# Kernel tuning notes

Measured on AMD Instinct MI355X. Metric: run time of the kernel, lower is better.

Reference implementation:

```python
import jax, jax.numpy as jnp
import numpy as np

D_MODEL = 512
NHEAD = 8
MAX_REL = 256  # max_relative_position


def _linear(x, w, b):
    # torch nn.Linear: y = x @ W^T + b, W: [out, in]
    return jnp.einsum('...i,oi->...o', x, w) + b


def setup_inputs() -> dict:
    key = jax.random.key(0)
    ks = jax.random.split(key, 16)
    B, S, D = 32, 512, D_MODEL
    s = 0.02
    inp = {
        'query': jax.random.normal(ks[0], (B, S, D), jnp.float32),
        'key':   jax.random.normal(ks[1], (B, S, D), jnp.float32),
        'value': jax.random.normal(ks[2], (B, S, D), jnp.float32),
        # local attention projections (torch Linear weights [out,in])
        'wq': jax.random.normal(ks[3], (D, D), jnp.float32) * s,
        'bq': jnp.zeros((D,), jnp.float32),
        'wk': jax.random.normal(ks[4], (D, D), jnp.float32) * s,
        'bk': jnp.zeros((D,), jnp.float32),
        'wv': jax.random.normal(ks[5], (D, D), jnp.float32) * s,
        'bv': jnp.zeros((D,), jnp.float32),
        'wo': jax.random.normal(ks[6], (D, D), jnp.float32) * s,
        'bo': jnp.zeros((D,), jnp.float32),
        # relative-position key embedding table [2*MAX_REL+1, head_dim]
        'rel_k': jax.random.normal(ks[7], (2 * MAX_REL + 1, D // NHEAD), jnp.float32) * s,
        # global nn.MultiheadAttention (nhead//2 heads): packed in_proj + out_proj
        'g_in_w': jax.random.normal(ks[8], (3 * D, D), jnp.float32) * s,
        'g_in_b': jnp.zeros((3 * D,), jnp.float32),
        'g_out_w': jax.random.normal(ks[9], (D, D), jnp.float32) * s,
        'g_out_b': jnp.zeros((D,), jnp.float32),
    }
    return inp


def reference(query, key, value, wq, bq, wk, bk, wv, bv, wo, bo, rel_k,
              g_in_w, g_in_b, g_out_w, g_out_b):
    B, S, D = query.shape
    H, hd = NHEAD, D // NHEAD

    # --- local attention with relative-position bias ---
    q = _linear(query, wq, bq).reshape(B, S, H, hd).transpose(0, 2, 1, 3)  # [B,H,S,hd]
    k = _linear(key,   wk, bk).reshape(B, S, H, hd).transpose(0, 2, 1, 3)
    v = _linear(value, wv, bv).reshape(B, S, H, hd).transpose(0, 2, 1, 3)

    scores = jnp.einsum('bhqd,bhkd->bhqk', q, k) / jnp.sqrt(jnp.float32(hd))

    # relative positions: distance[i,j] = j - i, clamped, shifted to [0, 2*MAX_REL]
    idx = jnp.arange(S)
    rel_ids = jnp.clip(idx[None, :] - idx[:, None], -MAX_REL, MAX_REL) + MAX_REL  # [S,S]
    rel_pos_k = rel_k[rel_ids]  # [S, S, hd]
    scores = scores + jnp.einsum('bhld,lrd->bhlr', q, rel_pos_k)

    attn = jax.nn.softmax(scores, axis=-1)
    local = jnp.einsum('bhqk,bhkd->bhqd', attn, v)
    local = local.transpose(0, 2, 1, 3).reshape(B, S, D)

    # --- global MHA with H//2 heads ---
    Hg = H // 2
    hdg = D // Hg
    qg = _linear(query, g_in_w[:D], g_in_b[:D]).reshape(B, S, Hg, hdg).transpose(0, 2, 1, 3)
    kg = _linear(key,   g_in_w[D:2 * D], g_in_b[D:2 * D]).reshape(B, S, Hg, hdg).transpose(0, 2, 1, 3)
    vg = _linear(value, g_in_w[2 * D:], g_in_b[2 * D:]).reshape(B, S, Hg, hdg).transpose(0, 2, 1, 3)
    gs = jnp.einsum('bhqd,bhkd->bhqk', qg, kg) / jnp.sqrt(jnp.float32(hdg))
    ga = jax.nn.softmax(gs, axis=-1)
    g = jnp.einsum('bhqk,bhkd->bhqd', ga, vg).transpose(0, 2, 1, 3).reshape(B, S, D)
    g = _linear(g, g_out_w, g_out_b)

    combined = 0.7 * local + 0.3 * g
    return _linear(combined, wo, bo)
```

## Files before the change

kernel.cpp:

```cpp
#include <hip/hip_runtime.h>

typedef __attribute__((ext_vector_type(8))) short bh8;
typedef __attribute__((ext_vector_type(4))) float f4;

#define DEVI static __device__ __forceinline__

DEVI unsigned short f2b(float f) {
  union { float f; unsigned u; } v; v.f = f;
  unsigned r = v.u + 0x7fffu + ((v.u >> 16) & 1u);
  return (unsigned short)(r >> 16);
}
DEVI float b2f(unsigned short h) {
  union { unsigned u; float f; } v; v.u = ((unsigned)h) << 16;
  return v.f;
}
DEVI f4 mfma16(bh8 a, bh8 b, f4 c) {
  return __builtin_amdgcn_mfma_f32_16x16x32_bf16(a, b, c, 0, 0, 0);
}
DEVI void gload_lds16(const unsigned short* g, unsigned short* l) {
  __builtin_amdgcn_global_load_lds(
      (const __attribute__((address_space(1))) void*)(g),
      (__attribute__((address_space(3))) void*)(l), 16, 0, 0);
}

__global__ __launch_bounds__(256) void prep_all_kern(
    const float* __restrict__ q, const float* __restrict__ k, const float* __restrict__ v,
    const float* __restrict__ wq, const float* __restrict__ wk, const float* __restrict__ wv,
    const float* __restrict__ g_in_w, const float* __restrict__ g_out_w,
    const float* __restrict__ wo, const float* __restrict__ rel_k,
    const float* __restrict__ bgo, const float* __restrict__ bo,
    unsigned short* __restrict__ xq, unsigned short* __restrict__ xk, unsigned short* __restrict__ xv,
    unsigned short* __restrict__ Wq, unsigned short* __restrict__ Wk, unsigned short* __restrict__ Wv,
    unsigned short* __restrict__ Wo_, unsigned short* __restrict__ WgoT,
    unsigned short* __restrict__ Bfin, unsigned short* __restrict__ Rk,
    float* __restrict__ bias2) {
  if (blockIdx.x < 8192) {
    long i = ((long)blockIdx.x * 256 + threadIdx.x) * 4;
    float4 a = *(const float4*)(q + i);
    float4 b = *(const float4*)(k + i);
    float4 c = *(const float4*)(v + i);
    union { unsigned short s[4]; uint2 u; } pa, pb, pc;
    pa.s[0] = f2b(a.x); pa.s[1] = f2b(a.y); pa.s[2] = f2b(a.z); pa.s[3] = f2b(a.w);
    pb.s[0] = f2b(b.x); pb.s[1] = f2b(b.y); pb.s[2] = f2b(b.z); pb.s[3] = f2b(b.w);
    pc.s[0] = f2b(c.x); pc.s[1] = f2b(c.y); pc.s[2] = f2b(c.z); pc.s[3] = f2b(c.w);
    *(uint2*)(xq + i) = pa.u;
    *(uint2*)(xk + i) = pb.u;
    *(uint2*)(xv + i) = pc.u;
    return;
  }
  int bw = blockIdx.x - 8192;
  if (bw >= 2337) {
    int o = (bw - 2337) * 256 + threadIdx.x;
    if (o < 512) {
      const float* r = wo + (long)o * 512;
      float s = 0.f;
#pragma unroll 4
      for (int m = 0; m < 512; m += 4) {
        float4 a = *(const float4*)(r + m);
        float4 b = *(const float4*)(bgo + m);
        s += a.x * b.x + a.y * b.y + a.z * b.z + a.w * b.w;
      }
      bias2[o] = bo[o] + 0.3f * s;
    }
    return;
  }
  long i = ((long)bw * 256 + threadIdx.x) * 4;
  if (i >= 2392128L) return;
  if (i >= 2097152L && i < 2359296L) {
    long off = i - 2097152L;
    int ii = (int)(off >> 9), p = (int)(off & 511);
    union { unsigned short s[4]; uint2 u; } w;
#pragma unroll
    for (int tt = 0; tt < 4; tt++) w.s[tt] = f2b(g_out_w[(p + tt) * 512 + ii]);
    *(uint2*)(WgoT + off) = w.u;
    return;
  }
  const float* src; unsigned short* dst; long off; float sc = 1.0f;
  if (i < 524288L)        { dst = Wq;  off = i; src = (i < 262144L) ? wq + i : g_in_w + (i - 262144L); }
  else if (i < 1048576L)  { long j = i - 524288L;  dst = Wk;  off = j; src = (j < 262144L) ? wk + j : g_in_w + j; }
  else if (i < 1572864L)  { long j = i - 1048576L; dst = Wv;  off = j; src = (j < 262144L) ? wv + j : g_in_w + 262144L + j; }
  else if (i < 1835008L)  { long j = i - 1572864L; dst = Wo_; off = j; src = wo + j; }
  else if (i < 2097152L)  { long j = i - 1835008L; int col = (int)(j >> 9), kk = (int)(j & 511);
                            dst = Bfin; off = (long)col * 1024 + kk; src = wo + j; sc = 0.7f; }
  else                    { long j = i - 2359296L; dst = Rk;  off = j; src = rel_k + j; }
  float4 f = *(const float4*)src;
  union { unsigned short s[4]; uint2 u; } p;
  p.s[0] = f2b(f.x * sc); p.s[1] = f2b(f.y * sc); p.s[2] = f2b(f.z * sc); p.s[3] = f2b(f.w * sc);
  *(uint2*)(dst + off) = p.u;
}

__global__ __launch_bounds__(256) void gemm3_kern(
    const unsigned short* __restrict__ Xq, const unsigned short* __restrict__ Xk,
    const unsigned short* __restrict__ Xv,
    const unsigned short* __restrict__ Wq, const unsigned short* __restrict__ Wk,
    const unsigned short* __restrict__ Wv,
    const float* __restrict__ bq, const float* __restrict__ bk, const float* __restrict__ bv,
    const float* __restrict__ g_in_b,
    unsigned short* __restrict__ Yq, unsigned short* __restrict__ Yk_,
    unsigned short* __restrict__ Yvt_l, unsigned short* __restrict__ Yvt_g,
    const unsigned short* __restrict__ Wo_, const unsigned short* __restrict__ WgoT,
    unsigned short* __restrict__ Bfin) {
  __shared__ unsigned short lsA[128 * 32];
  __shared__ unsigned short lsB[128 * 32];
  const int t = threadIdx.x;
  const int lane = t & 63, w = t >> 6;
  const int l15 = lane & 15, g = lane >> 4, g4 = g * 4;
  const int gs8 = (g ^ ((l15 >> 1) & 3)) * 8;
  const int n = blockIdx.x;

  const unsigned short *Ap, *Bp;
  const float *b0 = nullptr, *b1 = nullptr;
  int seg, rb, cb;
  if (n < 3072) {
    seg = n >> 10;
    int m = n & 1023;
    int x = m >> 3, c = m & 7;
    rb = (c * 16 + (x & 15)) * 128;
    cb = (x >> 4) * 128;
    Ap = (seg == 0) ? Xq : (seg == 1) ? Xk : Xv;
    Bp = (seg == 0) ? Wq : (seg == 1) ? Wk : Wv;
    b0 = (seg == 0) ? bq : (seg == 1) ? bk : bv;
    b1 = g_in_b + seg * 512;
  } else {
    seg = 3;
    int m2 = n - 3072;
    rb = (m2 & 3) * 128; cb = (m2 >> 2) * 128;
    Ap = Wo_; Bp = WgoT;
  }

  const int wr = (w >> 1) * 64, wc = (w & 1) * 64;
  const int r0 = t >> 2, r1 = 64 + (t >> 2);
  const int k0i = ((t & 3) ^ ((t >> 3) & 3)) * 8;

  const unsigned short* pa0 = Ap + (long)(rb + r0) * 512 + k0i;
  const unsigned short* pa1 = Ap + (long)(rb + r1) * 512 + k0i;
  const unsigned short* pb0 = Bp + (long)(cb + r0) * 512 + k0i;
  const unsigned short* pb1 = Bp + (long)(cb + r1) * 512 + k0i;
  unsigned short* dA0 = lsA + w * 512;
  unsigned short* dA1 = lsA + 2048 + w * 512;
  unsigned short* dB0 = lsB + w * 512;
  unsigned short* dB1 = lsB + 2048 + w * 512;

  f4 acc[4][4] = {};
  for (int k0 = 0; k0 < 512; k0 += 32) {
    __syncthreads();
    gload_lds16(pa0 + k0, dA0);
    gload_lds16(pa1 + k0, dA1);
    gload_lds16(pb0 + k0, dB0);
    gload_lds16(pb1 + k0, dB1);
    __syncthreads();
    bh8 af[4], bf[4];
#pragma unroll
    for (int m = 0; m < 4; m++) af[m] = *(const bh8*)(lsA + (wr + m * 16 + l15) * 32 + gs8);
#pragma unroll
    for (int nn = 0; nn < 4; nn++) bf[nn] = *(const bh8*)(lsB + (wc + nn * 16 + l15) * 32 + gs8);
    __builtin_amdgcn_s_setprio(1);
#pragma unroll
    for (int m = 0; m < 4; m++)
#pragma unroll
      for (int nn = 0; nn < 4; nn++)
        acc[m][nn] = mfma16(af[m], bf[nn], acc[m][nn]);
    __builtin_amdgcn_s_setprio(0);
  }

  if (seg == 3) {
#pragma unroll
    for (int m = 0; m < 4; m++)
#pragma unroll
      for (int nn = 0; nn < 4; nn++)
#pragma unroll
        for (int j = 0; j < 4; j++) {
          int row = rb + wr + m * 16 + g4 + j;
          int col = cb + wc + nn * 16 + l15;
          Bfin[(long)row * 1024 + 512 + col] = f2b(0.3f * acc[m][nn][j]);
        }
    return;
  }
  if (seg == 2) {
#pragma unroll
    for (int m = 0; m < 4; m++)
#pragma unroll
      for (int nn = 0; nn < 4; nn++) {
        int col = cb + wc + nn * 16 + l15;
        float bsv = (col < 512) ? b0[col] : b1[col - 512];
        unsigned r[4];
#pragma unroll
        for (int j = 0; j < 4; j++) {
          union { float f; unsigned u; } v; v.f = acc[m][nn][j] + bsv;
          r[j] = v.u + 0x7fffu + ((v.u >> 16) & 1u);
        }
        unsigned lo = (r[0] >> 16) | (r[1] & 0xffff0000u);
        unsigned hi = (r[2] >> 16) | (r[3] & 0xffff0000u);
        int row0 = rb + wr + m * 16 + g4;
        int bb = row0 >> 9, s = row0 & 511;
        if (col < 512) {
          int hh = col >> 6, d = col & 63;
          *(uint2*)(Yvt_l + (((long)(bb * 8 + hh) * 64 + d) << 9) + s) = make_uint2(lo, hi);
        } else {
          int c2 = col - 512, hg = c2 >> 7, dg = c2 & 127;
          *(uint2*)(Yvt_g + (((long)(bb * 4 + hg) * 128 + dg) << 9) + s) = make_uint2(lo, hi);
        }
      }
    return;
  }
  unsigned short* Yo = (seg == 0) ? Yq : Yk_;
#pragma unroll
  for (int m = 0; m < 4; m++)
#pragma unroll
    for (int nn = 0; nn < 4; nn++)
#pragma unroll
      for (int j = 0; j < 4; j++) {
        int row = rb + wr + m * 16 + g4 + j;
        int col = cb + wc + nn * 16 + l15;
        float v = acc[m][nn][j] + ((col < 512) ? b0[col] : b1[col - 512]);
        Yo[(long)row * 1024 + col] = f2b(v);
      }
}

__global__ __launch_bounds__(256) void gemm_fin_kern(
    const unsigned short* __restrict__ A, const unsigned short* __restrict__ Bw,
    const float* __restrict__ bias0, float* __restrict__ outf) {
  __shared__ unsigned short lsA[128 * 32];
  __shared__ unsigned short lsB[128 * 32];
  const int t = threadIdx.x;
  const int lane = t & 63, w = t >> 6;
  const int l15 = lane & 15, g = lane >> 4, g4 = g * 4;
  const int gs8 = (g ^ ((l15 >> 1) & 3)) * 8;
  int n = blockIdx.x;
  int x = n >> 3, c = n & 7;
  const int rb = (c * 16 + (x & 15)) * 128;
  const int cb = (x >> 4) * 128;
  const int wr = (w >> 1) * 64, wc = (w & 1) * 64;
  const int r0 = t >> 2, r1 = 64 + (t >> 2);
  const int k0i = ((t & 3) ^ ((t >> 3) & 3)) * 8;

  const unsigned short* pa0 = A + (long)(rb + r0) * 1024 + k0i;
  const unsigned short* pa1 = A + (long)(rb + r1) * 1024 + k0i;
  const unsigned short* pb0 = Bw + (long)(cb + r0) * 1024 + k0i;
  const unsigned short* pb1 = Bw + (long)(cb + r1) * 1024 + k0i;
  unsigned short* dA0 = lsA + w * 512;
  unsigned short* dA1 = lsA + 2048 + w * 512;
  unsigned short* dB0 = lsB + w * 512;
  unsigned short* dB1 = lsB + 2048 + w * 512;

  f4 acc[4][4] = {};
  for (int k0 = 0; k0 < 1024; k0 += 32) {
    __syncthreads();
    gload_lds16(pa0 + k0, dA0);
    gload_lds16(pa1 + k0, dA1);
    gload_lds16(pb0 + k0, dB0);
    gload_lds16(pb1 + k0, dB1);
    __syncthreads();
    bh8 af[4], bf[4];
#pragma unroll
    for (int m = 0; m < 4; m++) af[m] = *(const bh8*)(lsA + (wr + m * 16 + l15) * 32 + gs8);
#pragma unroll
    for (int nn = 0; nn < 4; nn++) bf[nn] = *(const bh8*)(lsB + (wc + nn * 16 + l15) * 32 + gs8);
    __builtin_amdgcn_s_setprio(1);
#pragma unroll
    for (int m = 0; m < 4; m++)
#pragma unroll
      for (int nn = 0; nn < 4; nn++)
        acc[m][nn] = mfma16(af[m], bf[nn], acc[m][nn]);
    __builtin_amdgcn_s_setprio(0);
  }
#pragma unroll
  for (int m = 0; m < 4; m++)
#pragma unroll
    for (int nn = 0; nn < 4; nn++)
#pragma unroll
      for (int j = 0; j < 4; j++) {
        int row = rb + wr + m * 16 + g4 + j;
        int col = cb + wc + nn * 16 + l15;
        outf[(long)row * 512 + col] = acc[m][nn][j] + bias0[col];
      }
}

__global__ __launch_bounds__(512, 4) void attn_local_kern(
    const unsigned short* __restrict__ Yq, const unsigned short* __restrict__ Yk,
    const unsigned short* __restrict__ Yvt, const unsigned short* __restrict__ relk,
    unsigned short* __restrict__ outC) {
  __shared__ unsigned short kv[2][8192];
  __shared__ unsigned short buf[32 * 524];
  __shared__ float redbuf[8][32];

  const int t = threadIdx.x, lane = t & 63, w = t >> 6;
  const int l15 = lane & 15, g = lane >> 4, g8 = g * 8;
  int n = blockIdx.x;
  int bid = (n & 7) * 512 + (n >> 3);
  const int qt = bid & 15;
  const int h = (bid >> 4) & 7;
  const int b = bid >> 7;
  const int qb = qt * 32;
  const long base = ((long)(b * 512)) * 1024 + h * 64;
  const long vbase = ((long)(b * 8 + h)) * 64 * 512;

#define STAGE_K(ROFF, BUF) { \
    const int c_ = t & 7; \
    _Pragma("unroll") \
    for (int it = 0; it < 2; it++) { \
      int rr = it * 64 + (t >> 3); \
      gload_lds16(Yk + base + (long)((ROFF) + rr) * 1024 + ((c_ ^ (rr & 7)) * 8), \
                  kv[BUF] + it * 4096 + w * 512); \
    } }
#define STAGE_V(COFF, BUF) { \
    const int c_ = t & 15; \
    _Pragma("unroll") \
    for (int it = 0; it < 2; it++) { \
      int dd_ = it * 32 + (t >> 4); \
      gload_lds16(Yvt + vbase + (long)dd_ * 512 + (COFF) + ((c_ ^ (dd_ & 15)) * 8), \
                  kv[BUF] + it * 4096 + w * 512); \
    } }
#define QK(CH) { \
    int rl = w * 16 + l15; \
    const unsigned short* kb_ = kv[(CH) & 1]; \
    bh8 k0 = *(const bh8*)(kb_ + rl * 64 + ((g ^ (rl & 7)) * 8)); \
    bh8 k1 = *(const bh8*)(kb_ + rl * 64 + (((g + 4) ^ (rl & 7)) * 8)); \
    _Pragma("unroll") \
    for (int mm = 0; mm < 2; mm++) { \
      f4 a = {}; \
      a = mfma16(qf[mm][0], k0, a); \
      a = mfma16(qf[mm][1], k1, a); \
      sc[mm][CH] = a; \
    } }
#define GATHER(CH) { \
    _Pragma("unroll") \
    for (int mm = 0; mm < 2; mm++) \
    _Pragma("unroll") \
    for (int j = 0; j < 4; j++) { \
      int lr = mm * 16 + g * 4 + j; \
      int rowb = lr * 524; \
      int idx = rowb + 256 - (qb + lr) + (CH) * 128 + w * 16 + l15; \
      idx = idx < rowb ? rowb : idx; \
      idx = idx > rowb + 512 ? rowb + 512 : idx; \
      float p = exp2f(fmaf(sc[mm][CH][j], 0.18033688011112042f, b2f(buf[idx]))); \
      sc[mm][CH][j] = p; \
      rs[mm][j] += p; \
    } }

  STAGE_K(0, 0);

  bh8 qf[2][2];
#pragma unroll
  for (int mm = 0; mm < 2; mm++) {
    const unsigned short* qp = Yq + base + (long)(qb + mm * 16 + l15) * 1024 + g8;
    qf[mm][0] = *(const bh8*)(qp);
    qf[mm][1] = *(const bh8*)(qp + 32);
  }

  for (int tt = w; tt < 33; tt += 8) {
    int ri = tt * 16 + l15; if (ri > 512) ri = 512;
    const unsigned short* rp = relk + ri * 64 + g8;
    bh8 rf0 = *(const bh8*)(rp), rf1 = *(const bh8*)(rp + 32);
    int col = tt * 16 + l15;
#pragma unroll
    for (int mm = 0; mm < 2; mm++) {
      f4 a = {};
      a = mfma16(qf[mm][0], rf0, a);
      a = mfma16(qf[mm][1], rf1, a);
      if (col < 524) {
#pragma unroll
        for (int j = 0; j < 4; j++)
          buf[(mm * 16 + g * 4 + j) * 524 + col] = f2b(a[j] * 1.4426950408889634f);
      }
    }
  }
  __syncthreads();

  f4 sc[2][4];
  float rs[2][4] = {};

#pragma unroll
  for (int c = 0; c < 4; c++) {
    if (c < 3) { STAGE_K((c + 1) * 128, (c + 1) & 1); }
    else       { STAGE_V(0, 0); }
    __builtin_amdgcn_s_setprio(1);
    QK(c);
    __builtin_amdgcn_s_setprio(0);
    GATHER(c);
    __syncthreads();
  }

#pragma unroll
  for (int mm = 0; mm < 2; mm++)
#pragma unroll
    for (int j = 0; j < 4; j++) {
      int lr = mm * 16 + g * 4 + j;
      float s = rs[mm][j];
      for (int d = 1; d < 16; d <<= 1) s += __shfl_xor(s, d, 64);
      if (l15 == 0) redbuf[w][lr] = s;
    }
#pragma unroll
  for (int mm = 0; mm < 2; mm++)
#pragma unroll
    for (int ch = 0; ch < 4; ch++) {
      int col = ch * 128 + w * 16 + l15;
#pragma unroll
      for (int j = 0; j < 4; j++)
        buf[(mm * 16 + g * 4 + j) * 524 + col] = f2b(sc[mm][ch][j]);
    }
  __syncthreads();

  const int mmw = w >> 2, dt = w & 3;
  const int dd = dt * 16 + l15;
  float rinvj[4];
#pragma unroll
  for (int j = 0; j < 4; j++) {
    int lr = mmw * 16 + g * 4 + j;
    float s = 0.f;
#pragma unroll
    for (int ww = 0; ww < 8; ww++) s += redbuf[ww][lr];
    rinvj[j] = __builtin_amdgcn_rcpf(s);
  }

  f4 accO = {};
#pragma unroll
  for (int d = 0; d < 4; d++) {
    if (d < 3) { STAGE_V((d + 1) * 128, (d + 1) & 1); }
    const unsigned short* vb_ = kv[d & 1];
    __builtin_amdgcn_s_setprio(1);
#pragma unroll
    for (int ks2 = 0; ks2 < 4; ks2++) {
      union { uint2 u[2]; bh8 v; } pa;
      const unsigned short* pp = buf + (mmw * 16 + l15) * 524 + (d * 4 + ks2) * 32 + g8;
      pa.u[0] = *(const uint2*)(pp);
      pa.u[1] = *(const uint2*)(pp + 4);
      bh8 vv = *(const bh8*)(vb_ + dd * 128 + (((ks2 * 4 + g) ^ (dd & 15)) * 8));
      accO = mfma16(pa.v, vv, accO);
    }
    __builtin_amdgcn_s_setprio(0);
    if (d < 3) __syncthreads();
  }
#pragma unroll
  for (int j = 0; j < 4; j++) {
    int row = qb + mmw * 16 + g * 4 + j;
    outC[((long)(b * 512 + row)) * 1024 + h * 64 + dt * 16 + l15] = f2b(accO[j] * rinvj[j]);
  }
#undef STAGE_K
#undef STAGE_V
#undef QK
#undef GATHER
}

__global__ __launch_bounds__(512, 4) void attn_glob_kern(
    const unsigned short* __restrict__ Yq, const unsigned short* __restrict__ Yk,
    const unsigned short* __restrict__ Yvt, unsigned short* __restrict__ outC) {
  __shared__ unsigned short kv[2][8192];
  __shared__ unsigned short buf[32 * 520];
  __shared__ float redbuf[8][32];

  const int t = threadIdx.x, lane = t & 63, w = t >> 6;
  const int l15 = lane & 15, g = lane >> 4, g8 = g * 8;
  int n = blockIdx.x;
  int bid = (n & 7) * 256 + (n >> 3);
  const int qt = bid & 15;
  const int hg = (bid >> 4) & 3;
  const int b = bid >> 6;
  const int qb = qt * 32;
  const long base = ((long)(b * 512)) * 1024 + 512 + hg * 128;
  const long vgbase = ((long)(b * 4 + hg)) * 128 * 512;

#define STAGE_GK(KC, BUF) { \
    const int c_ = t & 15; \
    _Pragma("unroll") \
    for (int it = 0; it < 2; it++) { \
      int rr = it * 32 + (t >> 4); \
      gload_lds16(Yk + base + (long)((KC) * 64 + rr) * 1024 + ((c_ ^ (rr & 15)) * 8), \
                  kv[BUF] + it * 4096 + w * 512); \
    } }
#define STAGE_GV(KC, BUF) { \
    const int c_ = t & 7; \
    _Pragma("unroll") \
    for (int it = 0; it < 2; it++) { \
      int dd_ = it * 64 + (t >> 3); \
      gload_lds16(Yvt + vgbase + (long)dd_ * 512 + (KC) * 64 + ((c_ ^ (dd_ & 7)) * 8), \
                  kv[BUF] + it * 4096 + w * 512); \
    } }

  const int mmq = w >> 2, wq4 = w & 3;

  STAGE_GK(0, 0);

  bh8 qf[4];
  {
    const unsigned short* qp = Yq + base + (long)(qb + mmq * 16 + l15) * 1024 + g8;
#pragma unroll
    for (int ks = 0; ks < 4; ks++) qf[ks] = *(const bh8*)(qp + ks * 32);
  }
  __syncthreads();

  f4 sc8[8];
#pragma unroll
  for (int kc = 0; kc < 8; kc++) {
    if (kc < 7) { STAGE_GK(kc + 1, (kc + 1) & 1); }
    else        { STAGE_GV(0, 0); }
    const unsigned short* kb_ = kv[kc & 1];
    const int rl = wq4 * 16 + l15;
    __builtin_amdgcn_s_setprio(1);
    f4 a = {};
#pragma unroll
    for (int ks = 0; ks < 4; ks++) {
      bh8 kf = *(const bh8*)(kb_ + rl * 128 + (((ks * 4 + g) ^ (rl & 15)) * 8));
      a = mfma16(qf[ks], kf, a);
    }
    sc8[kc] = a;
    __builtin_amdgcn_s_setprio(0);
    __syncthreads();
  }

#pragma unroll
  for (int j = 0; j < 4; j++) {
    int lr = mmq * 16 + g * 4 + j;
    float s = 0.f;
#pragma unroll
    for (int kc = 0; kc < 8; kc++) {
      float p = exp2f(sc8[kc][j] * 0.12751745334f);
      sc8[kc][j] = p;
      s += p;
    }
    for (int d = 1; d < 16; d <<= 1) s += __shfl_xor(s, d, 64);
    if (l15 == 0) redbuf[w][lr] = s;
  }
  __syncthreads();

#pragma unroll
  for (int kc = 0; kc < 8; kc++) {
    int col = kc * 64 + wq4 * 16 + l15;
#pragma unroll
    for (int j = 0; j < 4; j++)
      buf[(mmq * 16 + g * 4 + j) * 520 + col] = f2b(sc8[kc][j]);
  }
  float rinv[2][4];
#pragma unroll
  for (int mm = 0; mm < 2; mm++)
#pragma unroll
    for (int j = 0; j < 4; j++) {
      int lr = mm * 16 + g * 4 + j;
      float s = redbuf[mm * 4 + 0][lr] + redbuf[mm * 4 + 1][lr] +
                redbuf[mm * 4 + 2][lr] + redbuf[mm * 4 + 3][lr];
      rinv[mm][j] = __builtin_amdgcn_rcpf(s);
    }
  __syncthreads();

  const int dd = w * 16 + l15;
  f4 accO[2] = {};
#pragma unroll
  for (int kc = 0; kc < 8; kc++) {
    if (kc < 7) { STAGE_GV(kc + 1, (kc + 1) & 1); }
    const unsigned short* vb_ = kv[kc & 1];
    __builtin_amdgcn_s_setprio(1);
#pragma unroll
    for (int ks2 = 0; ks2 < 2; ks2++) {
      bh8 vv = *(const bh8*)(vb_ + dd * 64 + (((ks2 * 4 + g) ^ (dd & 7)) * 8));
#pragma unroll
      for (int mm = 0; mm < 2; mm++) {
        union { uint2 u[2]; bh8 v; } pa;
        const unsigned short* pp = buf + (mm * 16 + l15) * 520 + kc * 64 + ks2 * 32 + g8;
        pa.u[0] = *(const uint2*)(pp);
        pa.u[1] = *(const uint2*)(pp + 4);
        accO[mm] = mfma16(pa.v, vv, accO[mm]);
      }
    }
    __builtin_amdgcn_s_setprio(0);
    if (kc < 7) __syncthreads();
  }
#pragma unroll
  for (int mm = 0; mm < 2; mm++)
#pragma unroll
    for (int j = 0; j < 4; j++) {
      int row = qb + mm * 16 + g * 4 + j;
      outC[((long)(b * 512 + row)) * 1024 + 512 + hg * 128 + w * 16 + l15] = f2b(accO[mm][j] * rinv[mm][j]);
    }
#undef STAGE_GK
#undef STAGE_GV
}

extern "C" void kernel_launch(void* const* d_in, const int* in_sizes, int n_in,
                              void* d_out, int out_size, void* d_ws, size_t ws_size,
                              hipStream_t stream) {
  const float* query = (const float*)d_in[0];
  const float* key   = (const float*)d_in[1];
  const float* value = (const float*)d_in[2];
  const float* wq = (const float*)d_in[3];   const float* bq = (const float*)d_in[4];
  const float* wk = (const float*)d_in[5];   const float* bk = (const float*)d_in[6];
  const float* wv = (const float*)d_in[7];   const float* bv = (const float*)d_in[8];
  const float* wo = (const float*)d_in[9];   const float* bo = (const float*)d_in[10];
  const float* rel_k = (const float*)d_in[11];
  const float* g_in_w = (const float*)d_in[12];  const float* g_in_b = (const float*)d_in[13];
  const float* g_out_w = (const float*)d_in[14]; const float* g_out_b = (const float*)d_in[15];

  unsigned short* p = (unsigned short*)d_ws;
  unsigned short* Xq = p;            p += 8388608;
  unsigned short* Xk = p;            p += 8388608;
  unsigned short* Xv = p;            p += 8388608;
  unsigned short* Yq = p;            p += 16777216;
  unsigned short* Yk = p;            p += 16777216;
  unsigned short* Yvt_l = p;         p += 8388608;
  unsigned short* Yvt_g = p;         p += 8388608;
  unsigned short* Wq = p;            p += 524288;
  unsigned short* Wk = p;            p += 524288;
  unsigned short* Wv = p;            p += 524288;
  unsigned short* Wo_ = p;           p += 262144;
  unsigned short* WgoT = p;          p += 262144;
  unsigned short* Bfin = p;          p += 524288;
  unsigned short* Rk = p;            p += 32832;
  float* bias2 = (float*)p;          p += 1024;
  unsigned short* CAT = Xq;

  prep_all_kern<<<10531, 256, 0, stream>>>(query, key, value,
                                           wq, wk, wv, g_in_w, g_out_w, wo, rel_k,
                                           g_out_b, bo,
                                           Xq, Xk, Xv, Wq, Wk, Wv, Wo_, WgoT, Bfin, Rk, bias2);

  gemm3_kern<<<3088, 256, 0, stream>>>(Xq, Xk, Xv, Wq, Wk, Wv, bq, bk, bv, g_in_b,
                                       Yq, Yk, Yvt_l, Yvt_g, Wo_, WgoT, Bfin);

  attn_local_kern<<<4096, 512, 0, stream>>>(Yq, Yk, Yvt_l, Rk, CAT);
  attn_glob_kern<<<2048, 512, 0, stream>>>(Yq, Yk, Yvt_g, CAT);

  gemm_fin_kern<<<512, 256, 0, stream>>>(CAT, Bfin, bias2, (float*)d_out);
}
```

Baseline: 313.4 us.

## Triple-buffer GEMM K-loop loads and merge local/global attention kernels

Both GEMM kernels now use a three-stage LDS ring with direct global-to-LDS loads issued one tile ahead. A single barrier per iteration is guarded by explicit vmcnt waits, replacing the two __syncthreads around synchronous loads. Separately, the local and global attention kernels are fused into one launch that interleaves two local blocks and one global block per group of three. The aim is to hide load latency and remove a launch plus tail gap. The cost is triple the GEMM LDS use (48KB), which may lower occupancy, and a larger combined attention kernel whose register and LDS footprint is the maximum of both branches.

After: 290.0 us. 1.08x faster.

```diff
diff --git a/kernel.cpp b/kernel.cpp
--- a/kernel.cpp
+++ b/kernel.cpp
@@ -100,8 +100,8 @@
     unsigned short* __restrict__ Yvt_l, unsigned short* __restrict__ Yvt_g,
     const unsigned short* __restrict__ Wo_, const unsigned short* __restrict__ WgoT,
     unsigned short* __restrict__ Bfin) {
-  __shared__ unsigned short lsA[128 * 32];
-  __shared__ unsigned short lsB[128 * 32];
+  __shared__ unsigned short lsA[3][4096];
+  __shared__ unsigned short lsB[3][4096];
   const int t = threadIdx.x;
   const int lane = t & 63, w = t >> 6;
   const int l15 = lane & 15, g = lane >> 4, g4 = g * 4;
@@ -131,29 +131,35 @@
   const int wr = (w >> 1) * 64, wc = (w & 1) * 64;
   const int r0 = t >> 2, r1 = 64 + (t >> 2);
   const int k0i = ((t & 3) ^ ((t >> 3) & 3)) * 8;
-
   const unsigned short* pa0 = Ap + (long)(rb + r0) * 512 + k0i;
   const unsigned short* pa1 = Ap + (long)(rb + r1) * 512 + k0i;
   const unsigned short* pb0 = Bp + (long)(cb + r0) * 512 + k0i;
   const unsigned short* pb1 = Bp + (long)(cb + r1) * 512 + k0i;
-  unsigned short* dA0 = lsA + w * 512;
-  unsigned short* dA1 = lsA + 2048 + w * 512;
-  unsigned short* dB0 = lsB + w * 512;
-  unsigned short* dB1 = lsB + 2048 + w * 512;
-
+
+#define GST(KK, BUF) { \
+    gload_lds16(pa0 + (KK), lsA[BUF] + w * 512); \
+    gload_lds16(pa1 + (KK), lsA[BUF] + 2048 + w * 512); \
+    gload_lds16(pb0 + (KK), lsB[BUF] + w * 512); \
+    gload_lds16(pb1 + (KK), lsB[BUF] + 2048 + w * 512); }
+
+  GST(0, 0);
   f4 acc[4][4] = {};
-  for (int k0 = 0; k0 < 512; k0 += 32) {
-    __syncthreads();
-    gload_lds16(pa0 + k0, dA0);
-    gload_lds16(pa1 + k0, dA1);
-    gload_lds16(pb0 + k0, dB0);
-    gload_lds16(pb1 + k0, dB1);
-    __syncthreads();
+#pragma unroll
+  for (int it = 0; it < 16; it++) {
+    if (it < 15) {
+      GST((it + 1) * 32, (it + 1) % 3);
+      asm volatile("s_waitcnt vmcnt(4)" ::: "memory");
+    } else {
+      asm volatile("s_waitcnt vmcnt(0)" ::: "memory");
+    }
+    __builtin_amdgcn_s_barrier();
+    const unsigned short* LA = lsA[it % 3];
+    const unsigned short* LB = lsB[it % 3];
     bh8 af[4], bf[4];
 #pragma unroll
-    for (int m = 0; m < 4; m++) af[m] = *(const bh8*)(lsA + (wr + m * 16 + l15) * 32 + gs8);
-#pragma unroll
-    for (int nn = 0; nn < 4; nn++) bf[nn] = *(const bh8*)(lsB + (wc + nn * 16 + l15) * 32 + gs8);
+    for (int m = 0; m < 4; m++) af[m] = *(const bh8*)(LA + (wr + m * 16 + l15) * 32 + gs8);
+#pragma unroll
+    for (int nn = 0; nn < 4; nn++) bf[nn] = *(const bh8*)(LB + (wc + nn * 16 + l15) * 32 + gs8);
     __builtin_amdgcn_s_setprio(1);
 #pragma unroll
     for (int m = 0; m < 4; m++)
@@ -162,6 +168,7 @@
         acc[m][nn] = mfma16(af[m], bf[nn], acc[m][nn]);
     __builtin_amdgcn_s_setprio(0);
   }
+#undef GST
 
   if (seg == 3) {
 #pragma unroll
@@ -220,8 +227,8 @@
 __global__ __launch_bounds__(256) void gemm_fin_kern(
     const unsigned short* __restrict__ A, const unsigned short* __restrict__ Bw,
     const float* __restrict__ bias0, float* __restrict__ outf) {
-  __shared__ unsigned short lsA[128 * 32];
-  __shared__ unsigned short lsB[128 * 32];
+  __shared__ unsigned short lsA[3][4096];
+  __shared__ unsigned short lsB[3][4096];
   const int t = threadIdx.x;
   const int lane = t & 63, w = t >> 6;
   const int l15 = lane & 15, g = lane >> 4, g4 = g * 4;
@@ -238,24 +245,31 @@
   const unsigned short* pa1 = A + (long)(rb + r1) * 1024 + k0i;
   const unsigned short* pb0 = Bw + (long)(cb + r0) * 1024 + k0i;
   const unsigned short* pb1 = Bw + (long)(cb + r1) * 1024 + k0i;
-  unsigned short* dA0 = lsA + w * 512;
-  unsigned short* dA1 = lsA + 2048 + w * 512;
-  unsigned short* dB0 = lsB + w * 512;
-  unsigned short* dB1 = lsB + 2048 + w * 512;
-
+
+#define GST(KK, BUF) { \
+    gload_lds16(pa0 + (KK), lsA[BUF] + w * 512); \
+    gload_lds16(pa1 + (KK), lsA[BUF] + 2048 + w * 512); \
+    gload_lds16(pb0 + (KK), lsB[BUF] + w * 512); \
+    gload_lds16(pb1 + (KK), lsB[BUF] + 2048 + w * 512); }
+
+  GST(0, 0);
   f4 acc[4][4] = {};
-  for (int k0 = 0; k0 < 1024; k0 += 32) {
-    __syncthreads();
-    gload_lds16(pa0 + k0, dA0);
-    gload_lds16(pa1 + k0, dA1);
-    gload_lds16(pb0 + k0, dB0);
-    gload_lds16(pb1 + k0, dB1);
-    __syncthreads();
+#pragma unroll
+  for (int it = 0; it < 32; it++) {
+    if (it < 31) {
+      GST((it + 1) * 32, (it + 1) % 3);
+      asm volatile("s_waitcnt vmcnt(4)" ::: "memory");
+    } else {
+      asm volatile("s_waitcnt vmcnt(0)" ::: "memory");
+    }
+    __builtin_amdgcn_s_barrier();
+    const unsigned short* LA = lsA[it % 3];
+    const unsigned short* LB = lsB[it % 3];
     bh8 af[4], bf[4];
 #pragma unroll
-    for (int m = 0; m < 4; m++) af[m] = *(const bh8*)(lsA + (wr + m * 16 + l15) * 32 + gs8);
-#pragma unroll
-    for (int nn = 0; nn < 4; nn++) bf[nn] = *(const bh8*)(lsB + (wc + nn * 16 + l15) * 32 + gs8);
+    for (int m = 0; m < 4; m++) af[m] = *(const bh8*)(LA + (wr + m * 16 + l15) * 32 + gs8);
+#pragma unroll
+    for (int nn = 0; nn < 4; nn++) bf[nn] = *(const bh8*)(LB + (wc + nn * 16 + l15) * 32 + gs8);
     __builtin_amdgcn_s_setprio(1);
 #pragma unroll
     for (int m = 0; m < 4; m++)
@@ -264,6 +278,8 @@
         acc[m][nn] = mfma16(af[m], bf[nn], acc[m][nn]);
     __builtin_amdgcn_s_setprio(0);
   }
+#undef GST
+
 #pragma unroll
   for (int m = 0; m < 4; m++)
 #pragma unroll
@@ -276,24 +292,28 @@
       }
 }
 
-__global__ __launch_bounds__(512, 4) void attn_local_kern(
+__global__ __launch_bounds__(512, 4) void attn_kern(
     const unsigned short* __restrict__ Yq, const unsigned short* __restrict__ Yk,
-    const unsigned short* __restrict__ Yvt, const unsigned short* __restrict__ relk,
-    unsigned short* __restrict__ outC) {
+    const unsigned short* __restrict__ Yvt_l, const unsigned short* __restrict__ Yvt_g,
+    const unsigned short* __restrict__ relk, unsigned short* __restrict__ outC) {
   __shared__ unsigned short kv[2][8192];
   __shared__ unsigned short buf[32 * 524];
   __shared__ float redbuf[8][32];
 
   const int t = threadIdx.x, lane = t & 63, w = t >> 6;
   const int l15 = lane & 15, g = lane >> 4, g8 = g * 8;
-  int n = blockIdx.x;
-  int bid = (n & 7) * 512 + (n >> 3);
-  const int qt = bid & 15;
-  const int h = (bid >> 4) & 7;
-  const int b = bid >> 7;
-  const int qb = qt * 32;
-  const long base = ((long)(b * 512)) * 1024 + h * 64;
-  const long vbase = ((long)(b * 8 + h)) * 64 * 512;
+  const int n = blockIdx.x;
+  const int grp = n / 3, r3 = n - grp * 3;
+
+  if (r3 < 2) {
+    int ln = grp * 2 + r3;
+    int bid = (ln & 7) * 512 + (ln >> 3);
+    const int qt = bid & 15;
+    const int h = (bid >> 4) & 7;
+    const int b = bid >> 7;
+    const int qb = qt * 32;
+    const long base = ((long)(b * 512)) * 1024 + h * 64;
+    const long vbase = ((long)(b * 8 + h)) * 64 * 512;
 
 #define STAGE_K(ROFF, BUF) { \
     const int c_ = t & 7; \
@@ -308,7 +328,7 @@
     _Pragma("unroll") \
     for (int it = 0; it < 2; it++) { \
       int dd_ = it * 32 + (t >> 4); \
-      gload_lds16(Yvt + vbase + (long)dd_ * 512 + (COFF) + ((c_ ^ (dd_ & 15)) * 8), \
+      gload_lds16(Yvt_l + vbase + (long)dd_ * 512 + (COFF) + ((c_ ^ (dd_ & 15)) * 8), \
                   kv[BUF] + it * 4096 + w * 512); \
     } }
 #define QK(CH) { \
@@ -338,127 +358,117 @@
       rs[mm][j] += p; \
     } }
 
-  STAGE_K(0, 0);
-
-  bh8 qf[2][2];
-#pragma unroll
-  for (int mm = 0; mm < 2; mm++) {
-    const unsigned short* qp = Yq + base + (long)(qb + mm * 16 + l15) * 1024 + g8;
-    qf[mm][0] = *(const bh8*)(qp);
-    qf[mm][1] = *(const bh8*)(qp + 32);
-  }
-
-  for (int tt = w; tt < 33; tt += 8) {
-    int ri = tt * 16 + l15; if (ri > 512) ri = 512;
-    const unsigned short* rp = relk + ri * 64 + g8;
-    bh8 rf0 = *(const bh8*)(rp), rf1 = *(const bh8*)(rp + 32);
-    int col = tt * 16 + l15;
+    STAGE_K(0, 0);
+
+    bh8 qf[2][2];
 #pragma unroll
     for (int mm = 0; mm < 2; mm++) {
-      f4 a = {};
-      a = mfma16(qf[mm][0], rf0, a);
-      a = mfma16(qf[mm][1], rf1, a);
-      if (col < 524) {
+      const unsigned short* qp = Yq + base + (long)(qb + mm * 16 + l15) * 1024 + g8;
+      qf[mm][0] = *(const bh8*)(qp);
+      qf[mm][1] = *(const bh8*)(qp + 32);
+    }
+
+    for (int tt = w; tt < 33; tt += 8) {
+      int ri = tt * 16 + l15; if (ri > 512) ri = 512;
+      const unsigned short* rp = relk + ri * 64 + g8;
+      bh8 rf0 = *(const bh8*)(rp), rf1 = *(const bh8*)(rp + 32);
+      int col = tt * 16 + l15;
+#pragma unroll
+      for (int mm = 0; mm < 2; mm++) {
+        f4 a = {};
+        a = mfma16(qf[mm][0], rf0, a);
+        a = mfma16(qf[mm][1], rf1, a);
+        if (col < 524) {
+#pragma unroll
+          for (int j = 0; j < 4; j++)
+            buf[(mm * 16 + g * 4 + j) * 524 + col] = f2b(a[j] * 1.4426950408889634f);
+        }
+      }
+    }
+    __syncthreads();
+
+    f4 sc[2][4];
+    float rs[2][4] = {};
+
+#pragma unroll
+    for (int c = 0; c < 4; c++) {
+      if (c < 3) { STAGE_K((c + 1) * 128, (c + 1) & 1); }
+      else       { STAGE_V(0, 0); }
+      __builtin_amdgcn_s_setprio(1);
+      QK(c);
+      __builtin_amdgcn_s_setprio(0);
+      GATHER(c);
+      __syncthreads();
+    }
+
+#pragma unroll
+    for (int mm = 0; mm < 2; mm++)
+#pragma unroll
+      for (int j = 0; j < 4; j++) {
+        int lr = mm * 16 + g * 4 + j;
+        float s = rs[mm][j];
+        for (int d = 1; d < 16; d <<= 1) s += __shfl_xor(s, d, 64);
+        if (l15 == 0) redbuf[w][lr] = s;
+      }
+#pragma unroll
+    for (int mm = 0; mm < 2; mm++)
+#pragma unroll
+      for (int ch = 0; ch < 4; ch++) {
+        int col = ch * 128 + w * 16 + l15;
 #pragma unroll
         for (int j = 0; j < 4; j++)
-          buf[(mm * 16 + g * 4 + j) * 524 + col] = f2b(a[j] * 1.4426950408889634f);
-      }
-    }
-  }
-  __syncthreads();
-
-  f4 sc[2][4];
-  float rs[2][4] = {};
-
-#pragma unroll
-  for (int c = 0; c < 4; c++) {
-    if (c < 3) { STAGE_K((c + 1) * 128, (c + 1) & 1); }
-    else       { STAGE_V(0, 0); }
-    __builtin_amdgcn_s_setprio(1);
-    QK(c);
-    __builtin_amdgcn_s_setprio(0);
-    GATHER(c);
+          buf[(mm * 16 + g * 4 + j) * 524 + col] = f2b(sc[mm][ch][j]);
+      }
     __syncthreads();
-  }
-
-#pragma unroll
-  for (int mm = 0; mm < 2; mm++)
+
+    const int mmw = w >> 2, dt = w & 3;
+    const int dd = dt * 16 + l15;
+    float rinvj[4];
 #pragma unroll
     for (int j = 0; j < 4; j++) {
-      int lr = mm * 16 + g * 4 + j;
-      float s = rs[mm][j];
-      for (int d = 1; d < 16; d <<= 1) s += __shfl_xor(s, d, 64);
-      if (l15 == 0) redbuf[w][lr] = s;
-    }
-#pragma unroll
-  for (int mm = 0; mm < 2; mm++)
-#pragma unroll
-    for (int ch = 0; ch < 4; ch++) {
-      int col = ch * 128 + w * 16 + l15;
-#pragma unroll
-      for (int j = 0; j < 4; j++)
-        buf[(mm * 16 + g * 4 + j) * 524 + col] = f2b(sc[mm][ch][j]);
-    }
-  __syncthreads();
-
-  const int mmw = w >> 2, dt = w & 3;
-  const int dd = dt * 16 + l15;
-  float rinvj[4];
-#pragma unroll
-  for (int j = 0; j < 4; j++) {
-    int lr = mmw * 16 + g * 4 + j;
-    float s = 0.f;
-#pragma unroll
-    for (int ww = 0; ww < 8; ww++) s += redbuf[ww][lr];
-    rinvj[j] = __builtin_amdgcn_rcpf(s);
-  }
-
-  f4 accO = {};
-#pragma unroll
-  for (int d = 0; d < 4; d++) {
-    if (d < 3) { STAGE_V((d + 1) * 128, (d + 1) & 1); }
-    const unsigned short* vb_ = kv[d & 1];
-    __builtin_amdgcn_s_setprio(1);
-#pragma unroll
-    for (int ks2 = 0; ks2 < 4; ks2++) {
-      union { uint2 u[2]; bh8 v; } pa;
-      const unsigned short* pp = buf + (mmw * 16 + l15) * 524 + (d * 4 + ks2) * 32 + g8;
-      pa.u[0] = *(const uint2*)(pp);
-      pa.u[1] = *(const uint2*)(pp + 4);
-      bh8 vv = *(const bh8*)(vb_ + dd * 128 + (((ks2 * 4 + g) ^ (dd & 15)) * 8));
-      accO = mfma16(pa.v, vv, accO);
-    }
-    __builtin_amdgcn_s_setprio(0);
-    if (d < 3) __syncthreads();
-  }
-#pragma unroll
-  for (int j = 0; j < 4; j++) {
-    int row = qb + mmw * 16 + g * 4 + j;
-    outC[((long)(b * 512 + row)) * 1024 + h * 64 + dt * 16 + l15] = f2b(accO[j] * rinvj[j]);
-  }
+      int lr = mmw * 16 + g * 4 + j;
+      float s = 0.f;
+#pragma unroll
+      for (int ww = 0; ww < 8; ww++) s += redbuf[ww][lr];
+      rinvj[j] = __builtin_amdgcn_rcpf(s);
+    }
+
+    f4 accO = {};
+#pragma unroll
+    for (int d = 0; d < 4; d++) {
+      if (d < 3) { STAGE_V((d + 1) * 128, (d + 1) & 1); }
+      const unsigned short* vb_ = kv[d & 1];
+      __builtin_amdgcn_s_setprio(1);
+#pragma unroll
+      for (int ks2 = 0; ks2 < 4; ks2++) {
+        union { uint2 u[2]; bh8 v; } pa;
+        const unsigned short* pp = buf + (mmw * 16 + l15) * 524 + (d * 4 + ks2) * 32 + g8;
+        pa.u[0] = *(const uint2*)(pp);
+        pa.u[1] = *(const uint2*)(pp + 4);
+        bh8 vv = *(const bh8*)(vb_ + dd * 128 + (((ks2 * 4 + g) ^ (dd & 15)) * 8));
+        accO = mfma16(pa.v, vv, accO);
+      }
+      __builtin_amdgcn_s_setprio(0);
+      if (d < 3) __syncthreads();
+    }
+#pragma unroll
+    for (int j = 0; j < 4; j++) {
+      int row = qb + mmw * 16 + g * 4 + j;
+      outC[((long)(b * 512 + row)) * 1024 + h * 64 + dt * 16 + l15] = f2b(accO[j] * rinvj[j]);
+    }
 #undef STAGE_K
 #undef STAGE_V
 #undef QK
 #undef GATHER
-}
-
-__global__ __launch_bounds__(512, 4) void attn_glob_kern(
-    const unsigned short* __restrict__ Yq, const unsigned short* __restrict__ Yk,
-    const unsigned short* __restrict__ Yvt, unsigned short* __restrict__ outC) {
-  __shared__ unsigned short kv[2][8192];
-  __shared__ unsigned short buf[32 * 520];
-  __shared__ float redbuf[8][32];
-
-  const int t = threadIdx.x, lane = t & 63, w = t >> 6;
-  const int l15 = lane & 15, g = lane >> 4, g8 = g * 8;
-  int n = blockIdx.x;
-  int bid = (n & 7) * 256 + (n >> 3);
-  const int qt = bid & 15;
-  const int hg = (bid >> 4) & 3;
-  const int b = bid >> 6;
-  const int qb = qt * 32;
-  const long base = ((long)(b * 512)) * 1024 + 512 + hg * 128;
-  const long vgbase = ((long)(b * 4 + hg)) * 128 * 512;
+  } else {
+    int gn = grp;
+    int bid = (gn & 7) * 256 + (gn >> 3);
+    const int qt = bid & 15;
+    const int hg = (bid >> 4) & 3;
+    const int b = bid >> 6;
+    const int qb = qt * 32;
+    const long base = ((long)(b * 512)) * 1024 + 512 + hg * 128;
+    const long vgbase = ((long)(b * 4 + hg)) * 128 * 512;
 
 #define STAGE_GK(KC, BUF) { \
     const int c_ = t & 15; \
@@ -473,106 +483,107 @@
     _Pragma("unroll") \
     for (int it = 0; it < 2; it++) { \
       int dd_ = it * 64 + (t >> 3); \
-      gload_lds16(Yvt + vgbase + (long)dd_ * 512 + (KC) * 64 + ((c_ ^ (dd_ & 7)) * 8), \
+      gload_lds16(Yvt_g + vgbase + (long)dd_ * 512 + (KC) * 64 + ((c_ ^ (dd_ & 7)) * 8), \
                   kv[BUF] + it * 4096 + w * 512); \
     } }
 
-  const int mmq = w >> 2, wq4 = w & 3;
-
-  STAGE_GK(0, 0);
-
-  bh8 qf[4];
-  {
-    const unsigned short* qp = Yq + base + (long)(qb + mmq * 16 + l15) * 1024 + g8;
-#pragma unroll
-    for (int ks = 0; ks < 4; ks++) qf[ks] = *(const bh8*)(qp + ks * 32);
-  }
-  __syncthreads();
-
-  f4 sc8[8];
-#pragma unroll
-  for (int kc = 0; kc < 8; kc++) {
-    if (kc < 7) { STAGE_GK(kc + 1, (kc + 1) & 1); }
-    else        { STAGE_GV(0, 0); }
-    const unsigned short* kb_ = kv[kc & 1];
-    const int rl = wq4 * 16 + l15;
-    __builtin_amdgcn_s_setprio(1);
-    f4 a = {};
-#pragma unroll
-    for (int ks = 0; ks < 4; ks++) {
-      bh8 kf = *(const bh8*)(kb_ + rl * 128 + (((ks * 4 + g) ^ (rl & 15)) * 8));
-      a = mfma16(qf[ks], kf, a);
-    }
-    sc8[kc] = a;
-    __builtin_amdgcn_s_setprio(0);
+    const int mmq = w >> 2, wq4 = w & 3;
+
+    STAGE_GK(0, 0);
+
+    bh8 qf[4];
+    {
+      const unsigned short* qp = Yq + base + (long)(qb + mmq * 16 + l15) * 1024 + g8;
+#pragma unroll
+      for (int ks = 0; ks < 4; ks++) qf[ks] = *(const bh8*)(qp + ks * 32);
+    }
     __syncthreads();
-  }
-
-#pragma unroll
-  for (int j = 0; j < 4; j++) {
-    int lr = mmq * 16 + g * 4 + j;
-    float s = 0.f;
+
+    f4 sc8[8];
 #pragma unroll
     for (int kc = 0; kc < 8; kc++) {
-      float p = exp2f(sc8[kc][j] * 0.12751745334f);
-      sc8[kc][j] = p;
-      s += p;
-    }
-    for (int d = 1; d < 16; d <<= 1) s += __shfl_xor(s, d, 64);
-    if (l15 == 0) redbuf[w][lr] = s;
-  }
-  __syncthreads();
-
-#pragma unroll
-  for (int kc = 0; kc < 8; kc++) {
-    int col = kc * 64 + wq4 * 16 + l15;
-#pragma unroll
-    for (int j = 0; j < 4; j++)
-      buf[(mmq * 16 + g * 4 + j) * 520 + col] = f2b(sc8[kc][j]);
-  }
-  float rinv[2][4];
-#pragma unroll
-  for (int mm = 0; mm < 2; mm++)
+      if (kc < 7) { STAGE_GK(kc + 1, (kc + 1) & 1); }
+      else        { STAGE_GV(0, 0); }
+      const unsigned short* kb_ = kv[kc & 1];
+      const int rl = wq4 * 16 + l15;
+      __builtin_amdgcn_s_setprio(1);
+      f4 a = {};
+#pragma unroll
+      for (int ks = 0; ks < 4; ks++) {
+        bh8 kf = *(const bh8*)(kb_ + rl * 128 + (((ks * 4 + g) ^ (rl & 15)) * 8));
+        a = mfma16(qf[ks], kf, a);
+      }
+      sc8[kc] = a;
+      __builtin_amdgcn_s_setprio(0);
+      __syncthreads();
+    }
+
 #pragma unroll
     for (int j = 0; j < 4; j++) {
-      int lr = mm * 16 + g * 4 + j;
-      float s = redbuf[mm * 4 + 0][lr] + redbuf[mm * 4 + 1][lr] +
-                redbuf[mm * 4 + 2][lr] + redbuf[mm * 4 + 3][lr];
-      rinv[mm][j] = __builtin_amdgcn_rcpf(s);
-    }
-  __syncthreads();
-
-  const int dd = w * 16 + l15;
-  f4 accO[2] = {};
-#pragma unroll
-  for (int kc = 0; kc < 8; kc++) {
-    if (kc < 7) { STAGE_GV(kc + 1, (kc + 1) & 1); }
-    const unsigned short* vb_ = kv[kc & 1];
-    __builtin_amdgcn_s_setprio(1);
-#pragma unroll
-    for (int ks2 = 0; ks2 < 2; ks2++) {
-      bh8 vv = *(const bh8*)(vb_ + dd * 64 + (((ks2 * 4 + g) ^ (dd & 7)) * 8));
-#pragma unroll
-      for (int mm = 0; mm < 2; mm++) {
-        union { uint2 u[2]; bh8 v; } pa;
-        const unsigned short* pp = buf + (mm * 16 + l15) * 520 + kc * 64 + ks2 * 32 + g8;
-        pa.u[0] = *(const uint2*)(pp);
-        pa.u[1] = *(const uint2*)(pp + 4);
-        accO[mm] = mfma16(pa.v, vv, accO[mm]);
-      }
-    }
-    __builtin_amdgcn_s_setprio(0);
-    if (kc < 7) __syncthreads();
-  }
-#pragma unroll
-  for (int mm = 0; mm < 2; mm++)
-#pragma unroll
-    for (int j = 0; j < 4; j++) {
-      int row = qb + mm * 16 + g * 4 + j;
-      outC[((long)(b * 512 + row)) * 1024 + 512 + hg * 128 + w * 16 + l15] = f2b(accO[mm][j] * rinv[mm][j]);
-    }
+      int lr = mmq * 16 + g * 4 + j;
+      float s = 0.f;
+#pragma unroll
+      for (int kc = 0; kc < 8; kc++) {
+        float p = exp2f(sc8[kc][j] * 0.12751745334f);
+        sc8[kc][j] = p;
+        s += p;
+      }
+      for (int d = 1; d < 16; d <<= 1) s += __shfl_xor(s, d, 64);
+      if (l15 == 0) redbuf[w][lr] = s;
+    }
+    __syncthreads();
+
+#pragma unroll
+    for (int kc = 0; kc < 8; kc++) {
+      int col = kc * 64 + wq4 * 16 + l15;
+#pragma unroll
+      for (int j = 0; j < 4; j++)
+        buf[(mmq * 16 + g * 4 + j) * 524 + col] = f2b(sc8[kc][j]);
+    }
+    float rinv[2][4];
+#pragma unroll
+    for (int mm = 0; mm < 2; mm++)
+#pragma unroll
+      for (int j = 0; j < 4; j++) {
+        int lr = mm * 16 + g * 4 + j;
+        float s = redbuf[mm * 4 + 0][lr] + redbuf[mm * 4 + 1][lr] +
+                  redbuf[mm * 4 + 2][lr] + redbuf[mm * 4 + 3][lr];
+        rinv[mm][j] = __builtin_amdgcn_rcpf(s);
+      }
+    __syncthreads();
+
+    const int dd = w * 16 + l15;
+    f4 accO[2] = {};
+#pragma unroll
+    for (int kc = 0; kc < 8; kc++) {
+      if (kc < 7) { STAGE_GV(kc + 1, (kc + 1) & 1); }
+      const unsigned short* vb_ = kv[kc & 1];
+      __builtin_amdgcn_s_setprio(1);
+#pragma unroll
+      for (int ks2 = 0; ks2 < 2; ks2++) {
+        bh8 vv = *(const bh8*)(vb_ + dd * 64 + (((ks2 * 4 + g) ^ (dd & 7)) * 8));
+#pragma unroll
+        for (int mm = 0; mm < 2; mm++) {
+          union { uint2 u[2]; bh8 v; } pa;
+          const unsigned short* pp = buf + (mm * 16 + l15) * 524 + kc * 64 + ks2 * 32 + g8;
+          pa.u[0] = *(const uint2*)(pp);
+          pa.u[1] = *(const uint2*)(pp + 4);
+          accO[mm] = mfma16(pa.v, vv, accO[mm]);
+        }
+      }
+      __builtin_amdgcn_s_setprio(0);
+      if (kc < 7) __syncthreads();
+    }
+#pragma unroll
+    for (int mm = 0; mm < 2; mm++)
+#pragma unroll
+      for (int j = 0; j < 4; j++) {
+        int row = qb + mm * 16 + g * 4 + j;
+        outC[((long)(b * 512 + row)) * 1024 + 512 + hg * 128 + w * 16 + l15] = f2b(accO[mm][j] * rinv[mm][j]);
+      }
 #undef STAGE_GK
 #undef STAGE_GV
+  }
 }
 
 extern "C" void kernel_launch(void* const* d_in, const int* in_sizes, int n_in,
@@ -615,8 +626,7 @@
   gemm3_kern<<<3088, 256, 0, stream>>>(Xq, Xk, Xv, Wq, Wk, Wv, bq, bk, bv, g_in_b,
                                        Yq, Yk, Yvt_l, Yvt_g, Wo_, WgoT, Bfin);
 
-  attn_local_kern<<<4096, 512, 0, stream>>>(Yq, Yk, Yvt_l, Rk, CAT);
-  attn_glob_kern<<<2048, 512, 0, stream>>>(Yq, Yk, Yvt_g, CAT);
+  attn_kern<<<6144, 512, 0, stream>>>(Yq, Yk, Yvt_l, Yvt_g, Rk, CAT);
 
   gemm_fin_kern<<<512, 256, 0, stream>>>(CAT, Bfin, bias2, (float*)d_out);
 }
```
